# Kernel optimization log

Hardware: AMD Instinct MI355X
Metric: run time of the kernel (lower is better)

Reference implementation:

```python
import jax, jax.numpy as jnp
import numpy as np

B, N, K = 4, 8192, 16
EMBED, HID, NCLS = 64, 128, 13
EPS = 1e-5


def _bn(x, g, b):
    # BatchNorm1d in training mode: stats over all points (B*N), per channel
    m = jnp.mean(x, axis=(0, 1), keepdims=True)
    v = jnp.var(x, axis=(0, 1), keepdims=True)
    return (x - m) * jax.lax.rsqrt(v + EPS) * g + b


def _knn_idx(pos, k):
    # pos: [B,N,3] -> k nearest neighbor indices per point (self excluded)
    sq = jnp.sum(pos * pos, -1)  # [B,N]
    d2 = sq[:, :, None] + sq[:, None, :] - 2.0 * jnp.einsum('bnd,bmd->bnm', pos, pos)
    n = pos.shape[1]
    d2 = d2 + jnp.eye(n, dtype=pos.dtype) * 1e10  # mask self (loop=False)
    _, idx = jax.lax.top_k(-d2, k)  # [B,N,k]
    return idx


def _pt_conv(x, pos, idx, w_lin, w_src, w_dst, pos_w, pos_b):
    # PyG PointTransformerConv: vector attention over neighbors (incl. self loop)
    Bc = x.shape[0]
    bidx = jnp.arange(Bc)[:, None, None]
    v = x @ w_lin          # value:  lin(x)
    a_src = x @ w_src      # lin_src(x)
    a_dst = x @ w_dst      # lin_dst(x)
    vj = v[bidx, idx]                      # [B,N,k1,C]
    aj = a_src[bidx, idx]                  # [B,N,k1,C]
    pj = pos[bidx, idx]                    # [B,N,k1,3]
    delta = (pos[:, :, None, :] - pj) @ pos_w + pos_b   # pos_nn(pos_i - pos_j)
    attn = jax.nn.softmax(a_dst[:, :, None, :] - aj + delta, axis=2)
    return jnp.sum(attn * (vj + delta), axis=2)  # sum aggregation


def setup_inputs() -> dict:
    key = jax.random.key(0)
    ks = jax.random.split(key, 20)

    def w(k, fan_in, fan_out):
        return (jax.random.normal(k, (fan_in, fan_out), jnp.float32) / np.sqrt(fan_in)).astype(jnp.float32)

    inp = {
        'points': jax.random.normal(ks[0], (B, N, 3), jnp.float32),
        'embed_w1': w(ks[1], 3, EMBED), 'embed_b1': jnp.zeros((EMBED,), jnp.float32),
        'bn1_g': jnp.ones((EMBED,), jnp.float32), 'bn1_b': jnp.zeros((EMBED,), jnp.float32),
        'embed_w2': w(ks[2], EMBED, EMBED), 'embed_b2': jnp.zeros((EMBED,), jnp.float32),
        'bne_g': jnp.ones((EMBED,), jnp.float32), 'bne_b': jnp.zeros((EMBED,), jnp.float32),
        'l0_lin': w(ks[3], EMBED, HID), 'l0_src': w(ks[4], EMBED, HID), 'l0_dst': w(ks[5], EMBED, HID),
        'l0_pos_w': w(ks[6], 3, HID), 'l0_pos_b': jnp.zeros((HID,), jnp.float32),
        'l0_bn_g': jnp.ones((HID,), jnp.float32), 'l0_bn_b': jnp.zeros((HID,), jnp.float32),
        'l1_lin': w(ks[7], HID, HID), 'l1_src': w(ks[8], HID, HID), 'l1_dst': w(ks[9], HID, HID),
        'l1_pos_w': w(ks[10], 3, HID), 'l1_pos_b': jnp.zeros((HID,), jnp.float32),
        'l1_bn_g': jnp.ones((HID,), jnp.float32), 'l1_bn_b': jnp.zeros((HID,), jnp.float32),
        'dec_w1': w(ks[11], HID, HID), 'dec_b1': jnp.zeros((HID,), jnp.float32),
        'dec_bn_g': jnp.ones((HID,), jnp.float32), 'dec_bn_b': jnp.zeros((HID,), jnp.float32),
        'dec_w2': w(ks[12], HID, NCLS), 'dec_b2': jnp.zeros((NCLS,), jnp.float32),
    }
    return inp


def reference(points, embed_w1, embed_b1, bn1_g, bn1_b, embed_w2, embed_b2,
              bne_g, bne_b,
              l0_lin, l0_src, l0_dst, l0_pos_w, l0_pos_b, l0_bn_g, l0_bn_b,
              l1_lin, l1_src, l1_dst, l1_pos_w, l1_pos_b, l1_bn_g, l1_bn_b,
              dec_w1, dec_b1, dec_bn_g, dec_bn_b, dec_w2, dec_b2):
    Bc, Nc, _ = points.shape
    # embedding MLP: Linear -> BN -> ReLU -> Linear, then BN -> ReLU
    h = points @ embed_w1 + embed_b1
    h = jax.nn.relu(_bn(h, bn1_g, bn1_b))
    h = h @ embed_w2 + embed_b2
    x = jax.nn.relu(_bn(h, bne_g, bne_b))
    # kNN graph (per batch), then append self loop (add_self_loops=True)
    idx = _knn_idx(points, K)
    self_idx = jnp.broadcast_to(jnp.arange(Nc)[None, :, None], (Bc, Nc, 1))
    idxf = jnp.concatenate([idx, self_idx], axis=-1)  # [B,N,K+1]
    x = jax.nn.relu(_bn(_pt_conv(x, points, idxf, l0_lin, l0_src, l0_dst, l0_pos_w, l0_pos_b), l0_bn_g, l0_bn_b))
    x = jax.nn.relu(_bn(_pt_conv(x, points, idxf, l1_lin, l1_src, l1_dst, l1_pos_w, l1_pos_b), l1_bn_g, l1_bn_b))
    # decoder MLP (dropout = identity at inference)
    h = jax.nn.relu(_bn(x @ dec_w1 + dec_b1, dec_bn_g, dec_bn_b))
    logits = h @ dec_w2 + dec_b2  # [B,N,num_classes]
    return logits
```

## Files before the change

kernel.cpp:

```cpp
#include <hip/hip_runtime.h>
#include <math.h>

#define BB 4
#define NN 8192
#define PP 32768
#define KNN 16

typedef float f32x2 __attribute__((ext_vector_type(2)));
typedef float f32x4 __attribute__((ext_vector_type(4)));

__device__ __forceinline__ f32x2 pk_mul(f32x2 a, f32x2 b) {
  f32x2 d; asm("v_pk_mul_f32 %0, %1, %2" : "=v"(d) : "v"(a), "v"(b)); return d;
}
__device__ __forceinline__ f32x2 pk_add(f32x2 a, f32x2 b) {
  f32x2 d; asm("v_pk_add_f32 %0, %1, %2" : "=v"(d) : "v"(a), "v"(b)); return d;
}

__global__ __launch_bounds__(256) void k_embed1(const float* __restrict__ pts,
    const float* __restrict__ w1, const float* __restrict__ b1, float* __restrict__ h1,
    float* __restrict__ gsum, float* __restrict__ gss)
{
  int tid = threadIdx.x;
  int c = tid & 63, g = tid >> 6;
  float wx = w1[c], wy = w1[64 + c], wz = w1[128 + c], bc = b1[c];
  int base = blockIdx.x * 256;
  float s = 0.f, ss = 0.f;
  #pragma unroll 4
  for (int i = 0; i < 64; ++i) {
    int p = base + g + i * 4;
    float px = pts[p*3+0], py = pts[p*3+1], pz = pts[p*3+2];
    float h = fmaf(pz, wz, fmaf(py, wy, fmaf(px, wx, bc)));
    h1[(size_t)p*64 + c] = h;
    s += h; ss = fmaf(h, h, ss);
  }
  __shared__ float ls[256], lq[256];
  ls[tid] = s; lq[tid] = ss;
  __syncthreads();
  if (tid < 64) {
    float a  = ls[tid] + ls[tid+64] + ls[tid+128] + ls[tid+192];
    float b2 = lq[tid] + lq[tid+64] + lq[tid+128] + lq[tid+192];
    atomicAdd(gsum + tid, a);
    atomicAdd(gss  + tid, b2);
  }
}

__global__ __launch_bounds__(256) void k_prep(const float* __restrict__ pts, float* __restrict__ pp)
{
  int t = blockIdx.x * 256 + threadIdx.x;
  int b = t >> 12, m = t & 4095;
  int c = m >> 4, l = m & 15;
  int jl = b * NN + c * 32 + l;
  int jh = jl + 16;
  float xl = pts[jl*3+0], yl = pts[jl*3+1], zl = pts[jl*3+2];
  float xh = pts[jh*3+0], yh = pts[jh*3+1], zh = pts[jh*3+2];
  float wl = __fadd_rn(__fadd_rn(__fmul_rn(xl,xl), __fmul_rn(yl,yl)), __fmul_rn(zl,zl));
  float wh = __fadd_rn(__fadd_rn(__fmul_rn(xh,xh), __fmul_rn(yh,yh)), __fmul_rn(zh,zh));
  float* o = pp + (size_t)t * 8;
  *(float4*)(o + 0) = make_float4(xl, xh, yl, yh);
  *(float4*)(o + 4) = make_float4(zl, zh, wl, wh);
}

template<int K, int COUT, bool STATS>
__global__ __launch_bounds__(256) void k_proj(const float* __restrict__ in,
    const float* __restrict__ gsumI, const float* __restrict__ gssI,
    const float* __restrict__ gamma, const float* __restrict__ beta,
    const float* __restrict__ W0, const float* __restrict__ W1, const float* __restrict__ W2,
    const float* __restrict__ B0, const float* __restrict__ B1, const float* __restrict__ B2,
    float* __restrict__ O0, float* __restrict__ O1, float* __restrict__ O2,
    float* __restrict__ gsumO, float* __restrict__ gssO)
{
  constexpr int PTS = 64;
  constexpr int CW = 8;
  constexpr int CG = COUT / CW;
  constexpr int PW = PTS * CG / 256;
  const float* W  = (blockIdx.y == 0) ? W0 : (blockIdx.y == 1) ? W1 : W2;
  const float* Bb = (blockIdx.y == 0) ? B0 : (blockIdx.y == 1) ? B1 : B2;
  float*       O  = (blockIdx.y == 0) ? O0 : (blockIdx.y == 1) ? O1 : O2;
  __shared__ float xs[PTS][K + 1];
  __shared__ float scs[K], shs[K];
  int tid = threadIdx.x;
  if (tid < K) {
    float mean = gsumI[tid] * (1.0f / PP);
    float var  = gssI[tid] * (1.0f / PP) - mean * mean;
    float s = gamma[tid] / sqrtf(var + 1e-5f);
    scs[tid] = s;
    shs[tid] = beta[tid] - mean * s;
  }
  __syncthreads();
  int pbase = blockIdx.x * PTS;
  constexpr int T4 = PTS * K / 4;
  for (int i = tid; i < T4; i += 256) {
    int p = i / (K/4), k = (i % (K/4)) * 4;
    float4 v = *(const float4*)(in + (size_t)(pbase + p)*K + k);
    v.x = fmaxf(fmaf(v.x, scs[k+0], shs[k+0]), 0.f);
    v.y = fmaxf(fmaf(v.y, scs[k+1], shs[k+1]), 0.f);
    v.z = fmaxf(fmaf(v.z, scs[k+2], shs[k+2]), 0.f);
    v.w = fmaxf(fmaf(v.w, scs[k+3], shs[k+3]), 0.f);
    xs[p][k+0] = v.x; xs[p][k+1] = v.y; xs[p][k+2] = v.z; xs[p][k+3] = v.w;
  }
  __syncthreads();
  int cg = tid % CG, pg = tid / CG;
  int c0 = cg * CW, p0 = pg * PW;
  float acc[PW][CW];
  #pragma unroll
  for (int i = 0; i < PW; ++i) {
    #pragma unroll
    for (int j = 0; j < CW; ++j) acc[i][j] = 0.f;
  }
  #pragma unroll 4
  for (int k = 0; k < K; ++k) {
    float4 wa = *(const float4*)(W + (size_t)k*COUT + c0);
    float4 wb = *(const float4*)(W + (size_t)k*COUT + c0 + 4);
    #pragma unroll
    for (int i = 0; i < PW; ++i) {
      float x = xs[p0 + i][k];
      acc[i][0] = fmaf(x, wa.x, acc[i][0]);
      acc[i][1] = fmaf(x, wa.y, acc[i][1]);
      acc[i][2] = fmaf(x, wa.z, acc[i][2]);
      acc[i][3] = fmaf(x, wa.w, acc[i][3]);
      acc[i][4] = fmaf(x, wb.x, acc[i][4]);
      acc[i][5] = fmaf(x, wb.y, acc[i][5]);
      acc[i][6] = fmaf(x, wb.z, acc[i][6]);
      acc[i][7] = fmaf(x, wb.w, acc[i][7]);
    }
  }
  float bj[CW];
  #pragma unroll
  for (int j = 0; j < CW; ++j) bj[j] = Bb ? Bb[c0 + j] : 0.f;
  float sj[CW], qj[CW];
  #pragma unroll
  for (int j = 0; j < CW; ++j) { sj[j] = 0.f; qj[j] = 0.f; }
  #pragma unroll
  for (int i = 0; i < PW; ++i) {
    float* op = O + (size_t)(pbase + p0 + i)*COUT + c0;
    float o0 = acc[i][0]+bj[0], o1 = acc[i][1]+bj[1], o2 = acc[i][2]+bj[2], o3 = acc[i][3]+bj[3];
    float o4 = acc[i][4]+bj[4], o5 = acc[i][5]+bj[5], o6 = acc[i][6]+bj[6], o7 = acc[i][7]+bj[7];
    *(float4*)(op)     = make_float4(o0, o1, o2, o3);
    *(float4*)(op + 4) = make_float4(o4, o5, o6, o7);
    if (STATS) {
      sj[0]+=o0; sj[1]+=o1; sj[2]+=o2; sj[3]+=o3; sj[4]+=o4; sj[5]+=o5; sj[6]+=o6; sj[7]+=o7;
      qj[0]=fmaf(o0,o0,qj[0]); qj[1]=fmaf(o1,o1,qj[1]); qj[2]=fmaf(o2,o2,qj[2]); qj[3]=fmaf(o3,o3,qj[3]);
      qj[4]=fmaf(o4,o4,qj[4]); qj[5]=fmaf(o5,o5,qj[5]); qj[6]=fmaf(o6,o6,qj[6]); qj[7]=fmaf(o7,o7,qj[7]);
    }
  }
  if (STATS) {
    #pragma unroll
    for (int off = CG; off < 64; off <<= 1) {
      #pragma unroll
      for (int j = 0; j < CW; ++j) {
        sj[j] += __shfl_xor(sj[j], off);
        qj[j] += __shfl_xor(qj[j], off);
      }
    }
    __shared__ float ws[4][COUT], wq[4][COUT];
    int wid = tid >> 6, lane = tid & 63;
    if (lane < CG) {
      #pragma unroll
      for (int j = 0; j < CW; ++j) { ws[wid][lane*CW+j] = sj[j]; wq[wid][lane*CW+j] = qj[j]; }
    }
    __syncthreads();
    if (tid < COUT) {
      float a  = ws[0][tid] + ws[1][tid] + ws[2][tid] + ws[3][tid];
      float b2 = wq[0][tid] + wq[1][tid] + wq[2][tid] + wq[3][tid];
      atomicAdd(gsumO + tid, a);
      atomicAdd(gssO  + tid, b2);
    }
  }
}

__global__ __launch_bounds__(256, 8) void k_knn(const float* __restrict__ pp, int* __restrict__ idxout)
{
  int tid = threadIdx.x;
  int lane = tid & 63;
  int l16 = lane & 15;
  int g64 = lane & 48;
  int wv = (blockIdx.x * 256 + tid) >> 6;
  int b  = wv >> 11;
  int qbase = (wv * 4) & (NN - 1);
  int qc = qbase >> 5;
  int qr = (qbase & 31) + (lane >> 4);
  const float* pb = pp + (size_t)b * (NN * 4);

  float qx, qy, qz, qw;
  {
    int qslot = qc * 16 + (qr & 15);
    int qh = (qr >> 4) & 1;
    const float* qp = pb + (size_t)qslot * 8 + qh;
    qx = qp[0]; qy = qp[2]; qz = qp[4]; qw = qp[6];
  }
  f32x2 qx2; qx2.x = qx; qx2.y = qx;
  f32x2 qy2; qy2.x = qy; qy2.y = qy;
  f32x2 qz2; qz2.x = qz; qz2.y = qz;
  f32x2 qw2; qw2.x = qw; qw2.y = qw;

  int addr_push = (lane + 1) << 2;
  int addr_tau  = (g64 + 15) << 2;

  float lval = 3.4e38f;
  int   lidx = 0;
  float tau  = 3.4e38f;

  auto half_pass = [&](float d2, int jbase) {
    unsigned long long bal = __ballot(d2 < tau);
    if (bal) {
      unsigned slice = (unsigned)(bal >> g64) & 0xffffu;
      while (__ballot(slice != 0)) {
        bool live = slice != 0;
        int src = __ffs((int)slice) - 1;
        slice &= slice - 1;
        int ab = (g64 + (src & 15)) << 2;
        float v = __uint_as_float(__builtin_amdgcn_ds_bpermute(ab, __float_as_uint(d2)));
        if (!live) v = 3.4e38f;
        int jc = jbase + src;
        float pv = __uint_as_float(__builtin_amdgcn_ds_permute(addr_push, __float_as_uint(lval)));
        int   pi = __builtin_amdgcn_ds_permute(addr_push, lidx);
        bool atpos = (l16 == 0) || (pv <= v);
        if (lval > v) {
          lval = atpos ? v  : pv;
          lidx = atpos ? jc : pi;
        }
      }
      tau = __uint_as_float(__builtin_amdgcn_ds_bpermute(addr_tau, __float_as_uint(lval)));
    }
  };

  const float* cp = pb + (size_t)l16 * 8;

  {
    f32x4 A  = *(const f32x4*)(cp + 0);
    f32x4 Bq = *(const f32x4*)(cp + 4);
    cp += 128;
    f32x2 xs = __builtin_shufflevector(A, A, 0, 1);
    f32x2 ys = __builtin_shufflevector(A, A, 2, 3);
    f32x2 zs = __builtin_shufflevector(Bq, Bq, 0, 1);
    f32x2 ws = __builtin_shufflevector(Bq, Bq, 2, 3);
    f32x2 dot = pk_add(pk_add(pk_mul(qx2, xs), pk_mul(qy2, ys)), pk_mul(qz2, zs));
    f32x2 s2  = pk_add(qw2, ws);
    f32x2 t2  = pk_add(dot, dot);
    float d2lo = __fsub_rn(s2.x, t2.x);
    float d2hi = __fsub_rn(s2.y, t2.y);
    if (qc == 0) {
      bool lo = qr < 16;
      int  tl = lo ? qr : qr - 16;
      if (l16 == tl) { if (lo) d2lo = 3.4e38f; else d2hi = 3.4e38f; }
    }
    float v = d2lo; int ix = l16;
    #pragma unroll
    for (int k = 2; k <= 16; k <<= 1) {
      #pragma unroll
      for (int j = k >> 1; j >= 1; j >>= 1) {
        float ov = __shfl_xor(v, j, 16);
        int   oi = __shfl_xor(ix, j, 16);
        bool up    = (l16 & k) == 0;
        bool lower = (l16 & j) == 0;
        bool lt = (ov < v) || (ov == v && oi < ix);
        if ((up == lower) ? lt : !lt) { v = ov; ix = oi; }
      }
    }
    lval = v; lidx = ix;
    tau = __uint_as_float(__builtin_amdgcn_ds_bpermute(addr_tau, __float_as_uint(lval)));
    half_pass(d2hi, 16);
  }

  for (int c = 1; c < 256; ++c) {
    f32x4 A  = *(const f32x4*)(cp + 0);
    f32x4 Bq = *(const f32x4*)(cp + 4);
    cp += 128;
    f32x2 xs = __builtin_shufflevector(A, A, 0, 1);
    f32x2 ys = __builtin_shufflevector(A, A, 2, 3);
    f32x2 zs = __builtin_shufflevector(Bq, Bq, 0, 1);
    f32x2 ws = __builtin_shufflevector(Bq, Bq, 2, 3);
    f32x2 dot = pk_add(pk_add(pk_mul(qx2, xs), pk_mul(qy2, ys)), pk_mul(qz2, zs));
    f32x2 s2  = pk_add(qw2, ws);
    f32x2 t2  = pk_add(dot, dot);
    float d2lo = __fsub_rn(s2.x, t2.x);
    float d2hi = __fsub_rn(s2.y, t2.y);
    if (c == qc) {
      bool lo = qr < 16;
      int  tl = lo ? qr : qr - 16;
      if (l16 == tl) { if (lo) d2lo = 3.4e38f; else d2hi = 3.4e38f; }
    }
    half_pass(d2lo, c * 32);
    half_pass(d2hi, c * 32 + 16);
  }

  idxout[(size_t)wv * 64 + lane] = lidx;
}

__global__ __launch_bounds__(256) void k_conv(const float* __restrict__ V, const float* __restrict__ S,
    const float* __restrict__ D, const float* __restrict__ pts, const int* __restrict__ idx,
    const float* __restrict__ pw, const float* __restrict__ pbv, float* __restrict__ Y,
    float* __restrict__ gsum, float* __restrict__ gss)
{
  int tid = threadIdx.x;
  int lane = tid & 63;
  int wid  = (blockIdx.x * 256 + tid) >> 6;
  int c0 = lane * 2;
  float2 w0  = *(const float2*)(pw + c0);
  float2 w1  = *(const float2*)(pw + 128 + c0);
  float2 w2  = *(const float2*)(pw + 256 + c0);
  float2 pb2 = *(const float2*)(pbv + c0);
  float st0 = 0.f, st1 = 0.f, sq0 = 0.f, sq1 = 0.f;
  for (int p = wid; p < PP; p += 4096) {
    int b = p >> 13, self = p & (NN - 1);
    const float* pbase = pts + (size_t)b * NN * 3;
    float pix = pbase[self*3+0], piy = pbase[self*3+1], piz = pbase[self*3+2];
    float2 di = *(const float2*)(D + (size_t)p*128 + c0);
    float m0 = -3.4e38f, m1 = -3.4e38f, l0 = 0.f, l1 = 0.f, a0 = 0.f, a1 = 0.f;
    for (int t = 0; t < 17; ++t) {
      int j = (t < 16) ? idx[p*KNN + t] : self;
      float dx = pix - pbase[j*3+0];
      float dy = piy - pbase[j*3+1];
      float dz = piz - pbase[j*3+2];
      size_t off = ((size_t)b * NN + j) * 128 + c0;
      float2 sj = *(const float2*)(S + off);
      float2 vj = *(const float2*)(V + off);
      float de0 = fmaf(dz, w2.x, fmaf(dy, w1.x, fmaf(dx, w0.x, pb2.x)));
      float de1 = fmaf(dz, w2.y, fmaf(dy, w1.y, fmaf(dx, w0.y, pb2.y)));
      float g0 = di.x - sj.x + de0;
      float g1 = di.y - sj.y + de1;
      float mn0 = fmaxf(m0, g0), mn1 = fmaxf(m1, g1);
      float cr0 = __expf(m0 - mn0), cr1 = __expf(m1 - mn1);
      float e0  = __expf(g0 - mn0), e1  = __expf(g1 - mn1);
      l0 = fmaf(l0, cr0, e0);
      l1 = fmaf(l1, cr1, e1);
      a0 = fmaf(a0, cr0, e0 * (vj.x + de0));
      a1 = fmaf(a1, cr1, e1 * (vj.y + de1));
      m0 = mn0; m1 = mn1;
    }
    float2 o; o.x = a0 / l0; o.y = a1 / l1;
    *(float2*)(Y + (size_t)p*128 + c0) = o;
    st0 += o.x; st1 += o.y;
    sq0 = fmaf(o.x, o.x, sq0); sq1 = fmaf(o.y, o.y, sq1);
  }
  __shared__ float cs[4][128], cq[4][128];
  int w = tid >> 6;
  cs[w][c0] = st0; cs[w][c0+1] = st1;
  cq[w][c0] = sq0; cq[w][c0+1] = sq1;
  __syncthreads();
  if (tid < 128) {
    float a  = cs[0][tid] + cs[1][tid] + cs[2][tid] + cs[3][tid];
    float b2 = cq[0][tid] + cq[1][tid] + cq[2][tid] + cq[3][tid];
    atomicAdd(gsum + tid, a);
    atomicAdd(gss  + tid, b2);
  }
}

__global__ __launch_bounds__(256) void k_dec2(const float* __restrict__ T,
    const float* __restrict__ gsumI, const float* __restrict__ gssI,
    const float* __restrict__ gamma, const float* __restrict__ beta,
    const float* __restrict__ W, const float* __restrict__ bias, float* __restrict__ out)
{
  __shared__ float xs[64][132];
  __shared__ float wt[13][128];
  __shared__ float scs[128], shs[128];
  int tid = threadIdx.x;
  int pb = blockIdx.x * 64;
  if (tid < 128) {
    float mean = gsumI[tid] * (1.0f / PP);
    float var  = gssI[tid] * (1.0f / PP) - mean * mean;
    float s = gamma[tid] / sqrtf(var + 1e-5f);
    scs[tid] = s;
    shs[tid] = beta[tid] - mean * s;
  }
  __syncthreads();
  for (int i = tid; i < 13 * 128; i += 256) {
    int cls = i >> 7, k = i & 127;
    wt[cls][k] = W[k*13 + cls];
  }
  for (int i = tid; i < 64 * 32; i += 256) {
    int p = i >> 5, k = (i & 31) * 4;
    float4 v = *(const float4*)(T + (size_t)(pb + p)*128 + k);
    v.x = fmaxf(fmaf(v.x, scs[k+0], shs[k+0]), 0.f);
    v.y = fmaxf(fmaf(v.y, scs[k+1], shs[k+1]), 0.f);
    v.z = fmaxf(fmaf(v.z, scs[k+2], shs[k+2]), 0.f);
    v.w = fmaxf(fmaf(v.w, scs[k+3], shs[k+3]), 0.f);
    xs[p][k+0] = v.x; xs[p][k+1] = v.y; xs[p][k+2] = v.z; xs[p][k+3] = v.w;
  }
  __syncthreads();
  for (int o = tid; o < 64 * 13; o += 256) {
    int p = o / 13, cls = o - p * 13;
    float acc = bias[cls];
    const float4* xr = (const float4*)&xs[p][0];
    const float4* wr = (const float4*)&wt[cls][0];
    #pragma unroll 8
    for (int k4 = 0; k4 < 32; ++k4) {
      float4 a = xr[k4], w = wr[k4];
      acc = fmaf(a.x, w.x, acc);
      acc = fmaf(a.y, w.y, acc);
      acc = fmaf(a.z, w.z, acc);
      acc = fmaf(a.w, w.w, acc);
    }
    out[(size_t)(pb + p)*13 + cls] = acc;
  }
}

extern "C" void kernel_launch(void* const* d_in, const int* in_sizes, int n_in,
                              void* d_out, int out_size, void* d_ws, size_t ws_size,
                              hipStream_t stream)
{
  const float* pts      = (const float*)d_in[0];
  const float* embed_w1 = (const float*)d_in[1];
  const float* embed_b1 = (const float*)d_in[2];
  const float* bn1_g    = (const float*)d_in[3];
  const float* bn1_b    = (const float*)d_in[4];
  const float* embed_w2 = (const float*)d_in[5];
  const float* embed_b2 = (const float*)d_in[6];
  const float* bne_g    = (const float*)d_in[7];
  const float* bne_b    = (const float*)d_in[8];
  const float* l0_lin   = (const float*)d_in[9];
  const float* l0_src   = (const float*)d_in[10];
  const float* l0_dst   = (const float*)d_in[11];
  const float* l0_pos_w = (const float*)d_in[12];
  const float* l0_pos_b = (const float*)d_in[13];
  const float* l0_bn_g  = (const float*)d_in[14];
  const float* l0_bn_b  = (const float*)d_in[15];
  const float* l1_lin   = (const float*)d_in[16];
  const float* l1_src   = (const float*)d_in[17];
  const float* l1_dst   = (const float*)d_in[18];
  const float* l1_pos_w = (const float*)d_in[19];
  const float* l1_pos_b = (const float*)d_in[20];
  const float* l1_bn_g  = (const float*)d_in[21];
  const float* l1_bn_b  = (const float*)d_in[22];
  const float* dec_w1   = (const float*)d_in[23];
  const float* dec_b1   = (const float*)d_in[24];
  const float* dec_bn_g = (const float*)d_in[25];
  const float* dec_bn_b = (const float*)d_in[26];
  const float* dec_w2   = (const float*)d_in[27];
  const float* dec_b2   = (const float*)d_in[28];

  char* ws = (char*)d_ws;
  const size_t MB = 1024 * 1024;
  float* h1  = (float*)(ws + 0);
  float* h2  = (float*)(ws + 8*MB);
  int*   idx = (int*)  (ws + 16*MB);
  float* v0  = (float*)(ws + 18*MB);
  float* s0  = (float*)(ws + 34*MB);
  float* d0  = (float*)(ws + 50*MB);
  float* y0  = (float*)(ws + 66*MB);
  float* y1  = (float*)(ws + 82*MB);
  float* tt  = (float*)(ws + 0);
  float* pairs8 = (float*)(ws + 18*MB);
  float* st  = (float*)(ws + 98*MB);
  float *sum1=st+0,    *ss1=st+64;
  float *sum2=st+256,  *ss2=st+320;
  float *sum3=st+512,  *ss3=st+640;
  float *sum4=st+1024, *ss4=st+1152;
  float *sum5=st+1536, *ss5=st+1664;

  hipMemsetAsync(st, 0, 2048 * sizeof(float), stream);

  k_prep<<<64, 256, 0, stream>>>(pts, pairs8);
  k_knn<<<2048, 256, 0, stream>>>(pairs8, idx);

  k_embed1<<<128, 256, 0, stream>>>(pts, embed_w1, embed_b1, h1, sum1, ss1);
  k_proj<64,64,true><<<dim3(512,1), 256, 0, stream>>>(h1, sum1, ss1, bn1_g, bn1_b,
      embed_w2, embed_w2, embed_w2, embed_b2, embed_b2, embed_b2, h2, h2, h2, sum2, ss2);

  k_proj<64,128,false><<<dim3(512,3), 256, 0, stream>>>(h2, sum2, ss2, bne_g, bne_b,
      l0_lin, l0_src, l0_dst, nullptr, nullptr, nullptr, v0, s0, d0, nullptr, nullptr);
  k_conv<<<1024, 256, 0, stream>>>(v0, s0, d0, pts, idx, l0_pos_w, l0_pos_b, y0, sum3, ss3);

  k_proj<128,128,false><<<dim3(512,3), 256, 0, stream>>>(y0, sum3, ss3, l0_bn_g, l0_bn_b,
      l1_lin, l1_src, l1_dst, nullptr, nullptr, nullptr, v0, s0, d0, nullptr, nullptr);
  k_conv<<<1024, 256, 0, stream>>>(v0, s0, d0, pts, idx, l1_pos_w, l1_pos_b, y1, sum4, ss4);

  k_proj<128,128,true><<<dim3(512,1), 256, 0, stream>>>(y1, sum4, ss4, l1_bn_g, l1_bn_b,
      dec_w1, dec_w1, dec_w1, dec_b1, dec_b1, dec_b1, tt, tt, tt, sum5, ss5);
  k_dec2<<<512, 256, 0, stream>>>(tt, sum5, ss5, dec_bn_g, dec_bn_b, dec_w2, dec_b2, (float*)d_out);
}
```

Before: 643.7 us.

## Sort points by Morton code so kNN scan starts near the query

Points are binned into a 32^3 grid, Morton-sorted per batch by histogram, scan and scatter, and the kNN brute-force scan then starts at the query's own chunk and wraps around. The intent is that the top-16 threshold tightens early, so far fewer candidates pass the ballot test and the costly insertion loop runs less. Ties are now broken on original index so results match regardless of order, and outputs are written through the permutation. This adds three small kernels, a memset and atomics, and extra index loads and permutes inside the kNN loop.

```diff
diff --git a/kernel.cpp b/kernel.cpp
--- a/kernel.cpp
+++ b/kernel.cpp
@@ -5,6 +5,8 @@
 #define NN 8192
 #define PP 32768
 #define KNN 16
+#define KINF 3.4e38f
+#define PADIDX 0x7fffffff
 
 typedef float f32x2 __attribute__((ext_vector_type(2)));
 typedef float f32x4 __attribute__((ext_vector_type(4)));
@@ -14,6 +16,14 @@
 }
 __device__ __forceinline__ f32x2 pk_add(f32x2 a, f32x2 b) {
   f32x2 d; asm("v_pk_add_f32 %0, %1, %2" : "=v"(d) : "v"(a), "v"(b)); return d;
+}
+
+__device__ __forceinline__ unsigned mspread(int v) {
+  unsigned x = (unsigned)v & 0x1F;
+  x = (x | x << 8) & 0x100F;
+  x = (x | x << 4) & 0x10C3;
+  x = (x | x << 2) & 0x1249;
+  return x;
 }
 
 __global__ __launch_bounds__(256) void k_embed1(const float* __restrict__ pts,
@@ -44,20 +54,60 @@
   }
 }
 
-__global__ __launch_bounds__(256) void k_prep(const float* __restrict__ pts, float* __restrict__ pp)
-{
-  int t = blockIdx.x * 256 + threadIdx.x;
-  int b = t >> 12, m = t & 4095;
-  int c = m >> 4, l = m & 15;
-  int jl = b * NN + c * 32 + l;
-  int jh = jl + 16;
-  float xl = pts[jl*3+0], yl = pts[jl*3+1], zl = pts[jl*3+2];
-  float xh = pts[jh*3+0], yh = pts[jh*3+1], zh = pts[jh*3+2];
-  float wl = __fadd_rn(__fadd_rn(__fmul_rn(xl,xl), __fmul_rn(yl,yl)), __fmul_rn(zl,zl));
-  float wh = __fadd_rn(__fadd_rn(__fmul_rn(xh,xh), __fmul_rn(yh,yh)), __fmul_rn(zh,zh));
-  float* o = pp + (size_t)t * 8;
-  *(float4*)(o + 0) = make_float4(xl, xh, yl, yh);
-  *(float4*)(o + 4) = make_float4(zl, zh, wl, wh);
+__global__ __launch_bounds__(256) void k_cell(const float* __restrict__ pts,
+    int* __restrict__ mcode, int* __restrict__ hist)
+{
+  int p = blockIdx.x * 256 + threadIdx.x;
+  int b = p >> 13;
+  float x = pts[p*3+0], y = pts[p*3+1], z = pts[p*3+2];
+  int cx = (int)floorf((x + 5.12f) * 3.125f);
+  int cy = (int)floorf((y + 5.12f) * 3.125f);
+  int cz = (int)floorf((z + 5.12f) * 3.125f);
+  cx = min(max(cx, 0), 31); cy = min(max(cy, 0), 31); cz = min(max(cz, 0), 31);
+  int m = (int)(mspread(cx) | (mspread(cy) << 1) | (mspread(cz) << 2));
+  mcode[p] = m;
+  atomicAdd(hist + b * 32768 + m, 1);
+}
+
+__global__ __launch_bounds__(1024) void k_scan(int* __restrict__ hist)
+{
+  __shared__ int ls[1024];
+  int b = blockIdx.x, t = threadIdx.x;
+  int* hb = hist + b * 32768;
+  int base = t * 32;
+  int loc[32];
+  int tot = 0;
+  #pragma unroll
+  for (int i = 0; i < 32; ++i) { loc[i] = hb[base + i]; tot += loc[i]; }
+  ls[t] = tot;
+  __syncthreads();
+  for (int off = 1; off < 1024; off <<= 1) {
+    int v = (t >= off) ? ls[t - off] : 0;
+    __syncthreads();
+    ls[t] += v;
+    __syncthreads();
+  }
+  int run = ls[t] - tot;
+  #pragma unroll
+  for (int i = 0; i < 32; ++i) { int c = loc[i]; hb[base + i] = run; run += c; }
+}
+
+__global__ __launch_bounds__(256) void k_scat(const float* __restrict__ pts,
+    const int* __restrict__ mcode, int* __restrict__ hist,
+    float* __restrict__ pp, int* __restrict__ jmv)
+{
+  int p = blockIdx.x * 256 + threadIdx.x;
+  int b = p >> 13, i = p & (NN - 1);
+  float x = pts[p*3+0], y = pts[p*3+1], z = pts[p*3+2];
+  float sq = __fadd_rn(__fadd_rn(__fmul_rn(x,x), __fmul_rn(y,y)), __fmul_rn(z,z));
+  int m = mcode[p];
+  int pos = atomicAdd(hist + b * 32768 + m, 1);
+  int c = pos >> 5, l = pos & 31;
+  int half = l >> 4;
+  int slot = c * 16 + (l & 15);
+  float* o = pp + (size_t)b * (NN * 4) + (size_t)slot * 8 + half;
+  o[0] = x; o[2] = y; o[4] = z; o[6] = sq;
+  jmv[b * 8192 + slot * 2 + half] = i;
 }
 
 template<int K, int COUT, bool STATS>
@@ -168,7 +218,8 @@
   }
 }
 
-__global__ __launch_bounds__(256, 8) void k_knn(const float* __restrict__ pp, int* __restrict__ idxout)
+__global__ __launch_bounds__(256, 8) void k_knn(const float* __restrict__ pp,
+    const int* __restrict__ jmv, int* __restrict__ idxout)
 {
   int tid = threadIdx.x;
   int lane = tid & 63;
@@ -179,14 +230,16 @@
   int qbase = (wv * 4) & (NN - 1);
   int qc = qbase >> 5;
   int qr = (qbase & 31) + (lane >> 4);
-  const float* pb = pp + (size_t)b * (NN * 4);
-
-  float qx, qy, qz, qw;
+  const float* pb  = pp  + (size_t)b * (NN * 4);
+  const int*   jmb = jmv + b * 8192;
+
+  float qx, qy, qz, qw; int jq;
   {
     int qslot = qc * 16 + (qr & 15);
     int qh = (qr >> 4) & 1;
     const float* qp = pb + (size_t)qslot * 8 + qh;
     qx = qp[0]; qy = qp[2]; qz = qp[4]; qw = qp[6];
+    jq = jmb[qslot * 2 + qh];
   }
   f32x2 qx2; qx2.x = qx; qx2.y = qx;
   f32x2 qy2; qy2.x = qy; qy2.y = qy;
@@ -196,12 +249,10 @@
   int addr_push = (lane + 1) << 2;
   int addr_tau  = (g64 + 15) << 2;
 
-  float lval = 3.4e38f;
-  int   lidx = 0;
-  float tau  = 3.4e38f;
-
-  auto half_pass = [&](float d2, int jbase) {
-    unsigned long long bal = __ballot(d2 < tau);
+  float lval = KINF; int lidx = PADIDX;
+  float tau  = KINF; int tauj = PADIDX;
+
+  auto half_pass = [&](unsigned long long bal, float d2, int jcand) {
     if (bal) {
       unsigned slice = (unsigned)(bal >> g64) & 0xffffu;
       while (__ballot(slice != 0)) {
@@ -209,27 +260,26 @@
         int src = __ffs((int)slice) - 1;
         slice &= slice - 1;
         int ab = (g64 + (src & 15)) << 2;
-        float v = __uint_as_float(__builtin_amdgcn_ds_bpermute(ab, __float_as_uint(d2)));
-        if (!live) v = 3.4e38f;
-        int jc = jbase + src;
+        float v  = __uint_as_float(__builtin_amdgcn_ds_bpermute(ab, __float_as_uint(d2)));
+        int   jv = __builtin_amdgcn_ds_bpermute(ab, jcand);
+        if (!live) { v = KINF; jv = PADIDX; }
         float pv = __uint_as_float(__builtin_amdgcn_ds_permute(addr_push, __float_as_uint(lval)));
         int   pi = __builtin_amdgcn_ds_permute(addr_push, lidx);
-        bool atpos = (l16 == 0) || (pv <= v);
-        if (lval > v) {
-          lval = atpos ? v  : pv;
-          lidx = atpos ? jc : pi;
-        }
+        bool movein = (lval > v) || (lval == v && lidx > jv);
+        bool atpos  = (l16 == 0) || (pv < v) || (pv == v && pi < jv);
+        if (movein) { lval = atpos ? v : pv; lidx = atpos ? jv : pi; }
       }
-      tau = __uint_as_float(__builtin_amdgcn_ds_bpermute(addr_tau, __float_as_uint(lval)));
+      tau  = __uint_as_float(__builtin_amdgcn_ds_bpermute(addr_tau, __float_as_uint(lval)));
+      tauj = __builtin_amdgcn_ds_bpermute(addr_tau, lidx);
     }
   };
 
-  const float* cp = pb + (size_t)l16 * 8;
-
   {
+    int sl = qc * 16 + l16;
+    const float* cp = pb + (size_t)sl * 8;
     f32x4 A  = *(const f32x4*)(cp + 0);
     f32x4 Bq = *(const f32x4*)(cp + 4);
-    cp += 128;
+    int2 jc2 = *(const int2*)(jmb + sl * 2);
     f32x2 xs = __builtin_shufflevector(A, A, 0, 1);
     f32x2 ys = __builtin_shufflevector(A, A, 2, 3);
     f32x2 zs = __builtin_shufflevector(Bq, Bq, 0, 1);
@@ -239,12 +289,12 @@
     f32x2 t2  = pk_add(dot, dot);
     float d2lo = __fsub_rn(s2.x, t2.x);
     float d2hi = __fsub_rn(s2.y, t2.y);
-    if (qc == 0) {
+    {
       bool lo = qr < 16;
       int  tl = lo ? qr : qr - 16;
-      if (l16 == tl) { if (lo) d2lo = 3.4e38f; else d2hi = 3.4e38f; }
-    }
-    float v = d2lo; int ix = l16;
+      if (l16 == tl) { if (lo) d2lo = KINF; else d2hi = KINF; }
+    }
+    float v = d2lo; int ix = jc2.x;
     #pragma unroll
     for (int k = 2; k <= 16; k <<= 1) {
       #pragma unroll
@@ -258,14 +308,20 @@
       }
     }
     lval = v; lidx = ix;
-    tau = __uint_as_float(__builtin_amdgcn_ds_bpermute(addr_tau, __float_as_uint(lval)));
-    half_pass(d2hi, 16);
-  }
-
-  for (int c = 1; c < 256; ++c) {
+    tau  = __uint_as_float(__builtin_amdgcn_ds_bpermute(addr_tau, __float_as_uint(lval)));
+    tauj = __builtin_amdgcn_ds_bpermute(addr_tau, lidx);
+    unsigned long long bhi = __ballot((d2hi < tau) || (d2hi == tau && jc2.y < tauj));
+    half_pass(bhi, d2hi, jc2.y);
+  }
+
+  int c = qc;
+  for (int k = 1; k < 256; ++k) {
+    c = (c + 1) & 255;
+    int sl = c * 16 + l16;
+    const float* cp = pb + (size_t)sl * 8;
     f32x4 A  = *(const f32x4*)(cp + 0);
     f32x4 Bq = *(const f32x4*)(cp + 4);
-    cp += 128;
+    int2 jc2 = *(const int2*)(jmb + sl * 2);
     f32x2 xs = __builtin_shufflevector(A, A, 0, 1);
     f32x2 ys = __builtin_shufflevector(A, A, 2, 3);
     f32x2 zs = __builtin_shufflevector(Bq, Bq, 0, 1);
@@ -275,16 +331,13 @@
     f32x2 t2  = pk_add(dot, dot);
     float d2lo = __fsub_rn(s2.x, t2.x);
     float d2hi = __fsub_rn(s2.y, t2.y);
-    if (c == qc) {
-      bool lo = qr < 16;
-      int  tl = lo ? qr : qr - 16;
-      if (l16 == tl) { if (lo) d2lo = 3.4e38f; else d2hi = 3.4e38f; }
-    }
-    half_pass(d2lo, c * 32);
-    half_pass(d2hi, c * 32 + 16);
-  }
-
-  idxout[(size_t)wv * 64 + lane] = lidx;
+    unsigned long long blo = __ballot((d2lo < tau) || (d2lo == tau && jc2.x < tauj));
+    half_pass(blo, d2lo, jc2.x);
+    unsigned long long bhi = __ballot((d2hi < tau) || (d2hi == tau && jc2.y < tauj));
+    half_pass(bhi, d2hi, jc2.y);
+  }
+
+  idxout[((size_t)b * NN + jq) * KNN + l16] = lidx;
 }
 
 __global__ __launch_bounds__(256) void k_conv(const float* __restrict__ V, const float* __restrict__ S,
@@ -441,6 +494,9 @@
   float* y1  = (float*)(ws + 82*MB);
   float* tt  = (float*)(ws + 0);
   float* pairs8 = (float*)(ws + 18*MB);
+  int*   hist  = (int*)(ws + 34*MB);
+  int*   mcode = (int*)(ws + 34*MB + 512*1024);
+  int*   jmv   = (int*)(ws + 34*MB + 640*1024);
   float* st  = (float*)(ws + 98*MB);
   float *sum1=st+0,    *ss1=st+64;
   float *sum2=st+256,  *ss2=st+320;
@@ -449,9 +505,12 @@
   float *sum5=st+1536, *ss5=st+1664;
 
   hipMemsetAsync(st, 0, 2048 * sizeof(float), stream);
-
-  k_prep<<<64, 256, 0, stream>>>(pts, pairs8);
-  k_knn<<<2048, 256, 0, stream>>>(pairs8, idx);
+  hipMemsetAsync(hist, 0, 4 * 32768 * sizeof(int), stream);
+
+  k_cell<<<128, 256, 0, stream>>>(pts, mcode, hist);
+  k_scan<<<4, 1024, 0, stream>>>(hist);
+  k_scat<<<128, 256, 0, stream>>>(pts, mcode, hist, pairs8, jmv);
+  k_knn<<<2048, 256, 0, stream>>>(pairs8, jmv, idx);
 
   k_embed1<<<128, 256, 0, stream>>>(pts, embed_w1, embed_b1, h1, sum1, ss1);
   k_proj<64,64,true><<<dim3(512,1), 256, 0, stream>>>(h1, sum1, ss1, bn1_g, bn1_b,
```

After: 725.2 us. 12.7% more time.
